# Optimization experiments

Measured on AMD Instinct MI355X. Metric: run time of the kernel, lower is better.

## Reference

```python
import jax, jax.numpy as jnp
import numpy as np

CUTOFF = 5.0
CUTOFF_ANGLE = 3.5
N = 25000
E = 800000
EA = 300000
T = 1600000
NBASIS = 8          # default radial basis size (bessel)
NBASIS_ANG = 8
DIM = 256
DIM_SRC = 64
DIM_DST = 32
DIM_ANGLE = 8
NMAX_ANGLE = 4
SPECIES_DIM = 16
NSPEC = 50


def bessel_basis(r, rc, n):
    # sin(k*pi*r/rc)/r Bessel-type radial basis, k=1..n  -> [E, n]
    x = r[:, None]
    k = jnp.arange(1, n + 1, dtype=r.dtype)[None, :] * (np.pi / rc)
    return jnp.sqrt(2.0 / rc) * jnp.sin(k * x) / x


def tssr2(x):
    # two-sided smooth square-root activation (identity inside |x|<=1)
    ax = jnp.abs(x)
    return jnp.where(ax <= 1.0, x, jnp.sign(x) * (2.0 * jnp.sqrt(jnp.maximum(ax, 1.0)) - 1.0))


def setup_inputs() -> dict:
    key = jax.random.key(0)
    ks = jax.random.split(key, 24)
    species = jax.random.randint(ks[0], (N,), 1, 17)
    edge_src = jax.random.randint(ks[1], (E,), 0, N)
    edge_dst = jax.random.randint(ks[2], (E,), 0, N)
    distances = 0.5 + jax.random.uniform(ks[3], (E,)) * (CUTOFF - 0.5)
    switch = 0.5 + 0.5 * jnp.cos(np.pi * distances / CUTOFF)
    angles = jax.random.uniform(ks[4], (T,)) * np.pi
    angle_src = jax.random.randint(ks[5], (T,), 0, EA)
    angle_dst = jax.random.randint(ks[6], (T,), 0, EA)
    central_atom = jax.random.randint(ks[7], (T,), 0, N)
    distances_angle = 0.5 + jax.random.uniform(ks[8], (EA,)) * (CUTOFF_ANGLE - 0.5)
    switch_angle = 0.5 + 0.5 * jnp.cos(np.pi * distances_angle / CUTOFF_ANGLE)
    s = lambda k, sh, scale: jax.random.normal(k, sh, jnp.float32) * scale
    din0 = SPECIES_DIM + DIM_SRC + NBASIS * DIM_DST + (NMAX_ANGLE + 1) * DIM_ANGLE  # 376
    din1 = DIM + DIM_SRC + NBASIS * DIM_DST + (NMAX_ANGLE + 1) * DIM_ANGLE          # 616
    return {
        'species': species, 'edge_src': edge_src, 'edge_dst': edge_dst,
        'distances': distances, 'switch': switch,
        'angles': angles, 'angle_src': angle_src, 'angle_dst': angle_dst,
        'central_atom': central_atom, 'distances_angle': distances_angle,
        'switch_angle': switch_angle,
        'species_table': s(ks[9], (NSPEC, SPECIES_DIM), 1.0),
        'W_si0': s(ks[10], (SPECIES_DIM, DIM_SRC + DIM_DST), SPECIES_DIM ** -0.5),
        'W_si1': s(ks[11], (DIM, DIM_SRC + DIM_DST), DIM ** -0.5),
        'W_da0': s(ks[12], (NBASIS_ANG, DIM_ANGLE), NBASIS_ANG ** -0.5),
        'W_da1': s(ks[13], (NBASIS_ANG, DIM_ANGLE), NBASIS_ANG ** -0.5),
        'W_mix0': s(ks[14], (din0, DIM), din0 ** -0.5),
        'b_mix0': jnp.zeros((DIM,), jnp.float32),
        'W_mix1': s(ks[15], (din1, DIM), din1 ** -0.5),
        'b_mix1': jnp.zeros((DIM,), jnp.float32),
    }


def reference(species, edge_src, edge_dst, distances, switch, angles, angle_src,
              angle_dst, central_atom, distances_angle, switch_angle,
              species_table, W_si0, W_si1, W_da0, W_da1,
              W_mix0, b_mix0, W_mix1, b_mix1):
    n_atoms = species.shape[0]
    # species encoding (learned/random table lookup)
    xi = species_table[species]                                   # [N, 16]
    # radial embeddings, smoothly switched at cutoff
    rb = bessel_basis(distances, CUTOFF, NBASIS) * switch[:, None]            # [E, 8]
    rba = bessel_basis(distances_angle, CUTOFF_ANGLE, NBASIS_ANG) * switch_angle[:, None]  # [EA, 8]
    # fourier angular features cos(n*theta), n=0..nmax_angle
    nvec = jnp.arange(NMAX_ANGLE + 1, dtype=angles.dtype)[None, :]
    xa = jnp.cos(nvec * angles[:, None])                          # [T, 5]
    for W_si, W_da, W_mix, b_mix in ((W_si0, W_da0, W_mix0, b_mix0),
                                     (W_si1, W_da1, W_mix1, b_mix1)):
        s = xi @ W_si                                             # [N, 96]
        si, si_dst = s[:, :DIM_SRC], s[:, DIM_SRC:]
        # radial message passing: outer(radial_basis, neighbor features) -> scatter-add
        mij = (rb[:, :, None] * si_dst[edge_dst][:, None, :]).reshape(rb.shape[0], -1)  # [E, 256]
        mi = jax.ops.segment_sum(mij, edge_src, num_segments=n_atoms)                   # [N, 256]
        # angular triplet features: pairwise vectors combined per angle
        da = rba @ W_da                                           # [EA, 8]
        dij = da[angle_src] * da[angle_dst]                       # [T, 8]
        ang = (xa[:, :, None] * dij[:, None, :]).reshape(xa.shape[0], -1)               # [T, 40]
        ami = jax.ops.segment_sum(ang, central_atom, num_segments=n_atoms)              # [N, 40]
        # mixing network + tssr2 mixing activation, residual when shapes match
        ei = jnp.concatenate([xi, si, mi, ami], axis=-1)
        dxi = tssr2(ei @ W_mix + b_mix)
        xi = xi + dxi if xi.shape[-1] == dxi.shape[-1] else dxi
    return xi
```

## Files before the change

kernel.cpp:

```cpp
#include <hip/hip_runtime.h>
#include <hip/hip_bf16.h>

typedef __hip_bfloat16 bf16;
typedef __bf16 bf8 __attribute__((ext_vector_type(8)));
typedef float  f4  __attribute__((ext_vector_type(4)));

#define N_ATOMS 25000
#define NE      800000
#define NEA     300000
#define NT      1600000
#define APB     64
#define NBUK    ((N_ATOMS + APB - 1) / APB)
#define PADB    512

#define DIN0  376
#define DIN1  616
#define DINP0 384
#define DINP1 640

#define EBLK ((NE + 4095) / 4096)
#define TBLK ((NT + 4095) / 4096)

#define NFRAG0 ((DINP0 / 32) * 16 * 64)
#define NFRAG1 ((DINP1 / 32) * 16 * 64)
#define NFRAGS (8 * 6 * 64)
#define WBLK   ((NFRAG0 + NFRAG1 + NFRAGS + 255) / 256)

#define S0BLK2 ((N_ATOMS * 120 + 511) / 512)
#define DABLK2 ((NEA + 1 + 511) / 512)

#define MIBLK ((N_ATOMS + 1) / 2)

__device__ __forceinline__ float tssr2f(float x) {
    float ax = fabsf(x);
    return (ax <= 1.f) ? x : copysignf(2.f * __builtin_sqrtf(ax) - 1.f, x);
}

__device__ __forceinline__ unsigned short f2bf_rn(float v) {
    unsigned int b = __float_as_uint(v);
    b += 0x7FFF + ((b >> 16) & 1);
    return (unsigned short)(b >> 16);
}
__device__ __forceinline__ float bf2f(unsigned short u) {
    return __uint_as_float(((unsigned int)u) << 16);
}

__device__ __forceinline__ void wprep_one(const float* __restrict__ W, bf8* __restrict__ Wf,
                                          int K, int N, int ntiles, int f) {
    int lane = f & 63;
    int ft = f >> 6;
    int tile = ft % ntiles;
    int chunk = ft / ntiles;
    int n = tile * 16 + (lane & 15);
    int kb = chunk * 32 + (lane >> 4) * 8;
    bf8 v;
#pragma unroll
    for (int j = 0; j < 8; j++) {
        int k = kb + j;
        v[j] = (__bf16)((k < K) ? W[k * N + n] : 0.f);
    }
    Wf[f] = v;
}

__global__ __launch_bounds__(256) void k_wc(const float* __restrict__ W0, bf8* __restrict__ Wf0,
                                            const float* __restrict__ W1, bf8* __restrict__ Wf1,
                                            const float* __restrict__ WS, bf8* __restrict__ WfS,
                                            const int* __restrict__ esrc, const int* __restrict__ cat,
                                            int* __restrict__ ebcnt, int* __restrict__ tbcnt) {
    int bid = blockIdx.x;
    int t = threadIdx.x;
    if (bid < WBLK) {
        int f = bid * 256 + t;
        if (f < NFRAG0) {
            wprep_one(W0, Wf0, DIN0, 256, 16, f);
        } else if (f < NFRAG0 + NFRAG1) {
            wprep_one(W1, Wf1, DIN1, 256, 16, f - NFRAG0);
        } else if (f < NFRAG0 + NFRAG1 + NFRAGS) {
            wprep_one(WS, WfS, 256, 96, 6, f - NFRAG0 - NFRAG1);
        }
        return;
    }
    bid -= WBLK;
    __shared__ int h[NBUK];
    for (int b = t; b < NBUK; b += 256) h[b] = 0;
    __syncthreads();
    bool isE = bid < EBLK;
    const int* key = isE ? esrc : cat;
    int n = isE ? NE : NT;
    int base = (isE ? bid : bid - EBLK) * 4096;
#pragma unroll
    for (int k = 0; k < 16; k++) {
        int idx = base + k * 256 + t;
        if (idx < n) atomicAdd(&h[key[idx] >> 6], 1);
    }
    __syncthreads();
    int* g = isE ? ebcnt : tbcnt;
    for (int b = t; b < NBUK; b += 256)
        if (h[b]) atomicAdd(&g[b], h[b]);
}

__global__ __launch_bounds__(512) void k_scanB(const int* cnt0, int* off0, int* cur0,
                                               const int* cnt1, int* off1, int* cur1) {
    const int* cnt = blockIdx.x ? cnt1 : cnt0;
    int* off = blockIdx.x ? off1 : off0;
    int* cur = blockIdx.x ? cur1 : cur0;
    __shared__ int sh[512];
    int t = threadIdx.x;
    int v = (t < NBUK) ? cnt[t] : 0;
    sh[t] = v;
    __syncthreads();
    for (int d = 1; d < 512; d <<= 1) {
        int a = (t >= d) ? sh[t - d] : 0;
        __syncthreads();
        sh[t] += a;
        __syncthreads();
    }
    int excl = sh[t] - v;
    if (t <= NBUK) { off[t] = excl; if (t < NBUK) cur[t] = excl; }
}

__global__ __launch_bounds__(512) void k_bpre(const float* __restrict__ eA,
                                              const float* __restrict__ eB,
                                              const int* __restrict__ eC,
                                              const int* __restrict__ ekey,
                                              int* __restrict__ egcur,
                                              float4* __restrict__ ebuk,
                                              const float* __restrict__ tA,
                                              const int* __restrict__ tB,
                                              const int* __restrict__ tC,
                                              const int* __restrict__ tkey,
                                              int* __restrict__ tgcur,
                                              float4* __restrict__ tbuk,
                                              const int* __restrict__ sp,
                                              const float* __restrict__ table,
                                              const float* __restrict__ Wsi,
                                              unsigned short* __restrict__ ei0,
                                              float* __restrict__ sd,
                                              const float* __restrict__ dist,
                                              const float* __restrict__ sw2,
                                              const float* __restrict__ Wda0,
                                              const float* __restrict__ Wda1,
                                              unsigned short* __restrict__ dah0,
                                              unsigned short* __restrict__ dah1) {
    int bid = blockIdx.x;
    int t = threadIdx.x;
    if (bid < EBLK + TBLK) {
        __shared__ int cnt[NBUK];
        __shared__ int rbase[NBUK];
        for (int b = t; b < NBUK; b += 512) cnt[b] = 0;
        __syncthreads();
        bool isE = bid < EBLK;
        const int* key = isE ? ekey : tkey;
        int n = isE ? NE : NT;
        int* gcur = isE ? egcur : tgcur;
        float4* buk = isE ? ebuk : tbuk;
        int base = (isE ? bid : (bid - EBLK)) * 4096;
        float4 pay[8];
        int bk[8], off[8];
#pragma unroll
        for (int k = 0; k < 8; k++) {
            int idx = base + k * 512 + t;
            bk[k] = -1;
            if (idx < n) {
                float4 p;
                if (isE) {
                    p.x = eA[idx];
                    p.y = eB[idx];
                    p.z = __int_as_float(eC[idx]);
                } else {
                    p.x = __cosf(tA[idx]);
                    p.y = __int_as_float(tB[idx]);
                    p.z = __int_as_float(tC[idx]);
                }
                int ky = key[idx];
                p.w = __int_as_float(ky);
                pay[k] = p;
                bk[k] = ky >> 6;
                off[k] = atomicAdd(&cnt[bk[k]], 1);
            }
        }
        __syncthreads();
        for (int b = t; b < NBUK; b += 512)
            if (cnt[b]) rbase[b] = atomicAdd(&gcur[b], cnt[b]);
        __syncthreads();
#pragma unroll
        for (int k = 0; k < 8; k++)
            if (bk[k] >= 0) buk[rbase[bk[k]] + off[k]] = pay[k];
    } else if (bid < EBLK + TBLK + S0BLK2) {
        int idx = (bid - EBLK - TBLK) * 512 + t;
        if (idx >= N_ATOMS * 120) return;
        int i = idx / 120;
        int c = idx - i * 120;
        if (c >= 112) {
            ei0[(size_t)i * DINP0 + 376 + (c - 112)] = 0;
            return;
        }
        int s = sp[i];
        if (c < 16) {
            ei0[(size_t)i * DINP0 + c] = f2bf_rn(table[s * 16 + c]);
        } else {
            int cc = c - 16;
            float acc = 0.f;
#pragma unroll
            for (int k = 0; k < 16; k++)
                acc += table[s * 16 + k] * Wsi[k * 96 + cc];
            if (cc < 64) ei0[(size_t)i * DINP0 + 16 + cc] = f2bf_rn(acc);
            else         sd[i * 32 + cc - 64]             = acc;
        }
    } else {
        int e = (bid - EBLK - TBLK - S0BLK2) * 512 + t;
        if (e > NEA) return;
        if (e == NEA) {
            uint4 z = make_uint4(0, 0, 0, 0);
            *(uint4*)&dah0[(size_t)e * 8] = z;
            *(uint4*)&dah1[(size_t)e * 8] = z;
            return;
        }
        float d = dist[e];
        float s = sw2[e];
        float rb[8];
#pragma unroll
        for (int n = 0; n < 8; n++)
            rb[n] = 0.7559289460f * __sinf((n + 1) * 0.8975979010f * d) / d * s;
        unsigned short h0[8], h1[8];
#pragma unroll
        for (int c = 0; c < 8; c++) {
            float a0 = 0.f, a1 = 0.f;
#pragma unroll
            for (int n = 0; n < 8; n++) {
                a0 += rb[n] * Wda0[n * 8 + c];
                a1 += rb[n] * Wda1[n * 8 + c];
            }
            h0[c] = f2bf_rn(a0);
            h1[c] = f2bf_rn(a1);
        }
        *(uint4*)&dah0[e * 8] = *(uint4*)h0;
        *(uint4*)&dah1[e * 8] = *(uint4*)h1;
    }
}

__global__ __launch_bounds__(256) void k_binB2(const int* __restrict__ ebkoff,
                                               const int* __restrict__ ebcnt,
                                               const float4* __restrict__ ebuk,
                                               float* __restrict__ erb,
                                               int* __restrict__ edi,
                                               int* __restrict__ ebase_g,
                                               int* __restrict__ epcnt_g,
                                               const int* __restrict__ tbkoff,
                                               const int* __restrict__ tbcnt,
                                               const float4* __restrict__ tbuk,
                                               float4* __restrict__ tpay,
                                               int* __restrict__ tbase_g,
                                               int* __restrict__ tpcnt_g) {
    bool isE = blockIdx.x < NBUK;
    int b = isE ? blockIdx.x : (blockIdx.x - NBUK);
    const int* bkoff = isE ? ebkoff : tbkoff;
    const int* bkcnt = isE ? ebcnt : tbcnt;
    const float4* buk = isE ? ebuk : tbuk;
    int* baseg = isE ? ebase_g : tbase_g;
    int* pcntg = isE ? epcnt_g : tpcnt_g;
    int lo = b * APB;
    int hi = min(lo + APB, N_ATOMS);
    int sbase = bkoff[b];
    int bc = bkcnt[b];
    int fb = sbase + b * PADB;
    __shared__ int cntA[APB];
    __shared__ int abase[APB];
    __shared__ int cur[APB];
    int t = threadIdx.x;
    if (t < APB) cntA[t] = 0;
    __syncthreads();
    for (int p = sbase + t; p < sbase + bc; p += 256) {
        int a = __float_as_int(((const float*)(buk + p))[3]);
        atomicAdd(&cntA[a - lo], 1);
    }
    __syncthreads();
    if (t == 0) {
        int run = fb;
        for (int k = 0; k < hi - lo; k++) {
            int pc = (cntA[k] + 7) & ~7;
            abase[k] = run;
            cur[k] = run;
            baseg[lo + k] = run;
            pcntg[lo + k] = pc;
            run += pc;
        }
    }
    __syncthreads();
    if (t < hi - lo) {
        int c = cntA[t];
        int pc = (c + 7) & ~7;
        int base = abase[t];
        if (isE) {
            float4 z = make_float4(0.f, 0.f, 0.f, 0.f);
            for (int s = base + c; s < base + pc; s++) {
                edi[s] = 0;
                *(float4*)&erb[(size_t)s * 8]     = z;
                *(float4*)&erb[(size_t)s * 8 + 4] = z;
            }
        } else {
            float4 pz = make_float4(0.f, __int_as_float(NEA), __int_as_float(NEA), 0.f);
            for (int s = base + c; s < base + pc; s++) tpay[s] = pz;
        }
    }
    __syncthreads();
    for (int p = sbase + t; p < sbase + bc; p += 256) {
        float4 pay = buk[p];
        int a = __float_as_int(pay.w);
        int k = a - lo;
        int slot = atomicAdd(&cur[k], 1);
        if (isE) {
            float d = pay.x, s2 = pay.y;
            float q = 0.6324555320f * s2 / d;
            float r[8];
#pragma unroll
            for (int nn = 0; nn < 8; nn++)
                r[nn] = q * __sinf((nn + 1) * 0.6283185307f * d);
            *(float4*)&erb[(size_t)slot * 8]     = make_float4(r[0], r[1], r[2], r[3]);
            *(float4*)&erb[(size_t)slot * 8 + 4] = make_float4(r[4], r[5], r[6], r[7]);
            edi[slot] = __float_as_int(pay.z);
        } else {
            tpay[slot] = pay;
        }
    }
}

__global__ __launch_bounds__(256) void k_s1(const unsigned short* __restrict__ ei1,
                                            const bf8* __restrict__ Wf,
                                            unsigned short* __restrict__ ei1o,
                                            float* __restrict__ sd) {
    __shared__ __align__(16) __bf16 Asg[4][64][8];
    int t = threadIdx.x;
    int w = t >> 6, lane = t & 63;
    int a0 = blockIdx.x * 64;

    int satom = a0 + (t >> 2);
    int k8 = (t & 3) * 8;
    const unsigned short* arow = &ei1[(size_t)satom * DINP1 + k8];
    bool aok = satom < N_ATOMS;
    int dw = (t >> 2) >> 4;
    int dl = ((t >> 2) & 15) | ((t & 3) << 4);
    __bf16* adst = &Asg[dw][dl][0];

    f4 acc[6];
#pragma unroll
    for (int j = 0; j < 6; j++) {
        f4 z = {0.f, 0.f, 0.f, 0.f};
        acc[j] = z;
    }

    for (int ch = 0; ch < 8; ch++) {
        uint4 v = make_uint4(0, 0, 0, 0);
        if (aok) v = *(const uint4*)(arow + ch * 32);
        __syncthreads();
        *(uint4*)adst = v;
        __syncthreads();
        bf8 afr = *(const bf8*)&Asg[w][lane][0];
        const bf8* wp = &Wf[(ch * 6) * 64 + lane];
#pragma unroll
        for (int tn = 0; tn < 6; tn++) {
            bf8 b = wp[tn * 64];
            acc[tn] = __builtin_amdgcn_mfma_f32_16x16x32_bf16(afr, b, acc[tn], 0, 0, 0);
        }
    }

    int nlo = lane & 15, q = lane >> 4;
#pragma unroll
    for (int r = 0; r < 4; r++) {
        int atom = a0 + w * 16 + q * 4 + r;
        if (atom < N_ATOMS) {
#pragma unroll
            for (int tn = 0; tn < 6; tn++) {
                int col = tn * 16 + nlo;
                float v = acc[tn][r];
                if (col < 64) ei1o[(size_t)atom * DINP1 + 256 + col] = f2bf_rn(v);
                else          sd[atom * 32 + col - 64] = v;
            }
        }
    }
    for (int z = t; z < 64 * 24; z += 256) {
        int za = a0 + z / 24;
        if (za < N_ATOMS) ei1o[(size_t)za * DINP1 + 616 + z % 24] = 0;
    }
}

__device__ __forceinline__ void ami_win(const float4 twA, const unsigned short* __restrict__ dah,
                                        int gmax, int jj, int c,
                                        float& a0, float& a1, float& a2, float& a3, float& a4) {
    float scv[8];
    unsigned short dAv[8], dBv[8];
#pragma unroll
    for (int g = 0; g < 8; g++) {
        if (g < gmax) {
            int sl = g * 8 + jj;
            scv[g] = __shfl(twA.x, sl, 64);
            int ea = __float_as_int(__shfl(twA.y, sl, 64));
            int eb = __float_as_int(__shfl(twA.z, sl, 64));
            dAv[g] = dah[ea * 8 + c];
            dBv[g] = dah[eb * 8 + c];
        }
    }
#pragma unroll
    for (int g = 0; g < 8; g++) {
        if (g < gmax) {
            float dij = bf2f(dAv[g]) * bf2f(dBv[g]);
            float c1 = scv[g];
            float c2 = __builtin_fmaf(2.f * c1, c1, -1.f);
            float c3 = __builtin_fmaf(2.f * c1, c2, -c1);
            float c4 = __builtin_fmaf(2.f * c1, c3, -c2);
            a0 += dij;
            a1 = __builtin_fmaf(c1, dij, a1);
            a2 = __builtin_fmaf(c2, dij, a2);
            a3 = __builtin_fmaf(c3, dij, a3);
            a4 = __builtin_fmaf(c4, dij, a4);
        }
    }
}

__global__ __launch_bounds__(256) void k_seg(const int* __restrict__ ebase,
                                             const int* __restrict__ epcnt,
                                             const float* __restrict__ erb,
                                             const int* __restrict__ edi,
                                             const float* __restrict__ sd,
                                             unsigned short* __restrict__ mo, int mstride,
                                             const int* __restrict__ tbase,
                                             const int* __restrict__ tpcnt,
                                             const float4* __restrict__ tpay,
                                             const unsigned short* __restrict__ dah,
                                             unsigned short* __restrict__ ao, int astride) {
    __shared__ float4 smi[2][64];
    __shared__ float  sam[2][5][8];
    int t = threadIdx.x;
    int wv = t >> 6, l = t & 63;
    int slot = wv >> 1;
    int p    = wv & 1;

    if ((int)blockIdx.x < MIBLK) {
        int i = blockIdx.x * 2 + slot;
        bool valid = (i < N_ATOMS);
        int pbeg = 0, pcnt = 0;
        if (valid) { pbeg = tbase[i]; pcnt = tpcnt[i]; }
        int jj = l >> 3, c = l & 7;
        float a0 = 0.f, a1 = 0.f, a2 = 0.f, a3 = 0.f, a4 = 0.f;

        if (pcnt > 0) {
            int nG = pcnt >> 3;
            if (pcnt <= 128) {
                int h0 = (nG + 1) >> 1;
                int gb = p ? h0 : 0;
                int myg = p ? (nG - h0) : h0;
                if (myg > 0) {
                    int tb = gb * 8;
                    float4 twA = tpay[pbeg + tb + min(l, myg * 8 - 1)];
                    ami_win(twA, dah, myg, jj, c, a0, a1, a2, a3, a4);
                }
            } else {
                int nW = (pcnt + 63) >> 6;
                for (int W = p; W < nW; W += 2) {
                    int wbase = W * 64;
                    int rem = pcnt - wbase;
                    int lim = min(rem, 64);
                    float4 twA = tpay[pbeg + wbase + min(l, rem - 1)];
                    ami_win(twA, dah, lim >> 3, jj, c, a0, a1, a2, a3, a4);
                }
            }
        }

#pragma unroll
        for (int msk = 8; msk <= 32; msk <<= 1) {
            a0 += __shfl_xor(a0, msk, 64);
            a1 += __shfl_xor(a1, msk, 64);
            a2 += __shfl_xor(a2, msk, 64);
            a3 += __shfl_xor(a3, msk, 64);
            a4 += __shfl_xor(a4, msk, 64);
        }
        if (p == 1 && l < 8) {
            sam[slot][0][l] = a0; sam[slot][1][l] = a1; sam[slot][2][l] = a2;
            sam[slot][3][l] = a3; sam[slot][4][l] = a4;
        }
        __syncthreads();
        if (valid && p == 0 && l < 8) {
            a0 += sam[slot][0][l]; a1 += sam[slot][1][l]; a2 += sam[slot][2][l];
            a3 += sam[slot][3][l]; a4 += sam[slot][4][l];
            unsigned short* o = &ao[(size_t)i * astride + c];
            o[0]  = f2bf_rn(a0);
            o[8]  = f2bf_rn(a1);
            o[16] = f2bf_rn(a2);
            o[24] = f2bf_rn(a3);
            o[32] = f2bf_rn(a4);
        }
    } else {
        int i = ((int)blockIdx.x - MIBLK) * 2 + slot;
        bool valid = (i < N_ATOMS);
        int pbeg = 0, pcnt = 0;
        if (valid) { pbeg = ebase[i]; pcnt = epcnt[i]; }
        int n = l >> 3, cb = (l & 7) * 4;
        float4 acc = make_float4(0.f, 0.f, 0.f, 0.f);

        if (pcnt > 0) {
            int nG = pcnt >> 3;
            int h0 = (nG + 1) >> 1;
            int gbeg = p ? h0 : 0;
            int gend = p ? nG : h0;
            if (pcnt <= 64) {
                int eWin = edi[pbeg + min(l, pcnt - 1)];
                if (gbeg < gend) {
                    float cA = erb[((size_t)pbeg + gbeg * 8) * 8 + l];
                    for (int g = gbeg; g < gend; g++) {
                        float4 v[8];
#pragma unroll
                        for (int j = 0; j < 8; j++) {
                            int eid = __shfl(eWin, g * 8 + j, 64);
                            v[j] = *(const float4*)&sd[eid * 32 + cb];
                        }
                        float cB = 0.f;
                        if (g + 1 < gend) cB = erb[((size_t)pbeg + g * 8 + 8) * 8 + l];
#pragma unroll
                        for (int j = 0; j < 8; j++) {
                            float rbj = __shfl(cA, j * 8 + n, 64);
                            acc.x += rbj * v[j].x; acc.y += rbj * v[j].y;
                            acc.z += rbj * v[j].z; acc.w += rbj * v[j].w;
                        }
                        if (g + 1 < gend) cA = cB;
                    }
                }
            } else {
                const int* dp = edi + pbeg;
                for (int g = gbeg; g < gend; g++) {
                    const float* rp = erb + ((size_t)pbeg + g * 8) * 8 + n;
                    float4 v[8];
#pragma unroll
                    for (int j = 0; j < 8; j++) {
                        int eid = dp[g * 8 + j];
                        v[j] = *(const float4*)&sd[eid * 32 + cb];
                    }
#pragma unroll
                    for (int j = 0; j < 8; j++) {
                        float rbj = rp[j * 8];
                        acc.x += rbj * v[j].x; acc.y += rbj * v[j].y;
                        acc.z += rbj * v[j].z; acc.w += rbj * v[j].w;
                    }
                }
            }
        }

        if (p == 1) smi[slot][l] = acc;
        __syncthreads();
        if (valid && p == 0) {
            float4 o = smi[slot][l];
            acc.x += o.x; acc.y += o.y; acc.z += o.z; acc.w += o.w;
            ushort4 pk = make_ushort4(f2bf_rn(acc.x), f2bf_rn(acc.y),
                                      f2bf_rn(acc.z), f2bf_rn(acc.w));
            *(ushort4*)&mo[(size_t)i * mstride + l * 4] = pk;
        }
    }
}

template <int LAYER>
__global__ __launch_bounds__(256) void k_gemm(const unsigned short* __restrict__ ei,
                                              const bf8* __restrict__ Wf,
                                              const float* __restrict__ bias,
                                              const unsigned short* __restrict__ skip,
                                              float* __restrict__ outf,
                                              unsigned short* __restrict__ outb) {
    constexpr int DINP = (LAYER == 0) ? DINP0 : DINP1;
    constexpr int NCH = DINP / 32;
    __shared__ __align__(16) __bf16 Asg[2][64][8];
    int t = threadIdx.x;
    int w = t >> 6, lane = t & 63;
    int a0 = blockIdx.x * 32;

    int f  = t * 4;
    int tA = f >> 9;
    int al = (f >> 3) & 63;
    int j0 = f & 7;
    int sm = al & 15, sq = al >> 4;
    int ga = a0 + tA * 16 + sm;
    const unsigned short* arow = &ei[(size_t)ga * DINP + sq * 8 + j0];
    __bf16* adst = &Asg[0][0][0] + f;
    bool aok = (ga < N_ATOMS);

    f4 acc[2][4];
#pragma unroll
    for (int i = 0; i < 2; i++)
#pragma unroll
        for (int j = 0; j < 4; j++) {
            f4 z = {0.f, 0.f, 0.f, 0.f};
            acc[i][j] = z;
        }

    for (int ch = 0; ch < NCH; ch++) {
        uint2 v = make_uint2(0, 0);
        if (aok) v = *(const uint2*)(arow + ch * 32);
        __syncthreads();
        *(uint2*)adst = v;
        __syncthreads();
        bf8 afr0 = *(const bf8*)&Asg[0][lane][0];
        bf8 afr1 = *(const bf8*)&Asg[1][lane][0];
        const bf8* wp = &Wf[(ch * 16 + w * 4) * 64 + lane];
#pragma unroll
        for (int tn = 0; tn < 4; tn++) {
            bf8 b = wp[tn * 64];
            acc[0][tn] = __builtin_amdgcn_mfma_f32_16x16x32_bf16(afr0, b, acc[0][tn], 0, 0, 0);
            acc[1][tn] = __builtin_amdgcn_mfma_f32_16x16x32_bf16(afr1, b, acc[1][tn], 0, 0, 0);
        }
    }

    int nlo = lane & 15, q = lane >> 4;
#pragma unroll
    for (int tA2 = 0; tA2 < 2; tA2++) {
#pragma unroll
        for (int r = 0; r < 4; r++) {
            int atom = a0 + tA2 * 16 + q * 4 + r;
            if (atom < N_ATOMS) {
#pragma unroll
                for (int tn = 0; tn < 4; tn++) {
                    int col = w * 64 + tn * 16 + nlo;
                    float vv = tssr2f(acc[tA2][tn][r] + bias[col]);
                    if (LAYER == 0) {
                        outb[(size_t)atom * DINP1 + col] = f2bf_rn(vv);
                    } else {
                        outf[(size_t)atom * 256 + col] =
                            vv + bf2f(skip[(size_t)atom * DINP1 + col]);
                    }
                }
            }
        }
    }
}

extern "C" void kernel_launch(void* const* d_in, const int* in_sizes, int n_in,
                              void* d_out, int out_size, void* d_ws, size_t ws_size,
                              hipStream_t stream) {
    const int*   species     = (const int*)d_in[0];
    const int*   edge_src    = (const int*)d_in[1];
    const int*   edge_dst    = (const int*)d_in[2];
    const float* distances   = (const float*)d_in[3];
    const float* sw          = (const float*)d_in[4];
    const float* angles      = (const float*)d_in[5];
    const int*   angle_src   = (const int*)d_in[6];
    const int*   angle_dst   = (const int*)d_in[7];
    const int*   central     = (const int*)d_in[8];
    const float* dist_a      = (const float*)d_in[9];
    const float* sw_a        = (const float*)d_in[10];
    const float* table       = (const float*)d_in[11];
    const float* W_si0       = (const float*)d_in[12];
    const float* W_si1       = (const float*)d_in[13];
    const float* W_da0       = (const float*)d_in[14];
    const float* W_da1       = (const float*)d_in[15];
    const float* W_mix0      = (const float*)d_in[16];
    const float* b_mix0      = (const float*)d_in[17];
    const float* W_mix1      = (const float*)d_in[18];
    const float* b_mix1      = (const float*)d_in[19];
    float* out = (float*)d_out;

    char* p = (char*)d_ws;
    auto alloc = [&](size_t bytes) {
        char* r = p;
        p += (bytes + 255) & ~(size_t)255;
        return (void*)r;
    };
    unsigned short* ei0 = (unsigned short*)alloc((size_t)N_ATOMS * DINP0 * 2);
    unsigned short* ei1 = (unsigned short*)alloc((size_t)N_ATOMS * DINP1 * 2);
    float*  sd   = (float*)alloc((size_t)N_ATOMS * 32 * 4);
    unsigned short* dah0 = (unsigned short*)alloc((size_t)(NEA + 1) * 8 * 2);
    unsigned short* dah1 = (unsigned short*)alloc((size_t)(NEA + 1) * 8 * 2);
    float*  erbf = (float*)alloc((size_t)(NE + NBUK * PADB) * 8 * 4);
    int*    edi  = (int*)alloc((size_t)(NE + NBUK * PADB) * 4);
    float4* tpay = (float4*)alloc((size_t)(NT + NBUK * PADB) * 16);
    float4* ebuk = (float4*)alloc((size_t)NE * 16);
    bf8*    Wf0  = (bf8*)alloc((size_t)NFRAG0 * 16);
    bf8*    Wf1  = (bf8*)alloc((size_t)NFRAG1 * 16);
    bf8*    WfS1 = (bf8*)alloc((size_t)NFRAGS * 16);
    int* ebase  = (int*)alloc((size_t)N_ATOMS * 4);
    int* epcnt  = (int*)alloc((size_t)N_ATOMS * 4);
    int* tbase  = (int*)alloc((size_t)N_ATOMS * 4);
    int* tpcnt  = (int*)alloc((size_t)N_ATOMS * 4);
    int* bcnt   = (int*)alloc((size_t)2 * NBUK * 4);
    int* ebkoff = (int*)alloc((size_t)(NBUK + 1) * 4);
    int* tbkoff = (int*)alloc((size_t)(NBUK + 1) * 4);
    int* gce    = (int*)alloc((size_t)NBUK * 4);
    int* gct    = (int*)alloc((size_t)NBUK * 4);
    (void)ws_size;
    int* ebcnt = bcnt;
    int* tbcnt = bcnt + NBUK;

    float4* tbuk = (float4*)ei1;

    hipMemsetAsync(bcnt, 0, (size_t)2 * NBUK * 4, stream);

    k_wc<<<WBLK + EBLK + TBLK, 256, 0, stream>>>(
        W_mix0, Wf0, W_mix1, Wf1, W_si1, WfS1,
        edge_src, central, ebcnt, tbcnt);

    k_scanB<<<2, 512, 0, stream>>>(ebcnt, ebkoff, gce, tbcnt, tbkoff, gct);

    k_bpre<<<EBLK + TBLK + S0BLK2 + DABLK2, 512, 0, stream>>>(
        distances, sw, edge_dst, edge_src, gce, ebuk,
        angles, angle_src, angle_dst, central, gct, tbuk,
        species, table, W_si0, ei0, sd,
        dist_a, sw_a, W_da0, W_da1, dah0, dah1);

    k_binB2<<<2 * NBUK, 256, 0, stream>>>(
        ebkoff, ebcnt, ebuk, erbf, edi, ebase, epcnt,
        tbkoff, tbcnt, tbuk, tpay, tbase, tpcnt);

    int gemm_grid = (N_ATOMS + 31) / 32;

    k_seg<<<2 * MIBLK, 256, 0, stream>>>(ebase, epcnt, erbf, edi, sd, ei0 + 80, DINP0,
                                         tbase, tpcnt, tpay, dah0, ei0 + 336, DINP0);
    k_gemm<0><<<gemm_grid, 256, 0, stream>>>(ei0, Wf0, b_mix0, nullptr, nullptr, ei1);

    k_s1<<<(N_ATOMS + 63) / 64, 256, 0, stream>>>(ei1, WfS1, ei1, sd);
    k_seg<<<2 * MIBLK, 256, 0, stream>>>(ebase, epcnt, erbf, edi, sd, ei1 + 320, DINP1,
                                         tbase, tpcnt, tpay, dah1, ei1 + 576, DINP1);
    k_gemm<1><<<gemm_grid, 256, 0, stream>>>(ei1, Wf1, b_mix1, ei1, out, nullptr);
}
```

Before: 401.0 us.

## Compute both layers' angular aggregates in one pass with packed triplet payloads

The angular triplet features do not depend on the atom state, so both layers' angular segment sums are now computed in the first segment-reduction launch. The second launch only does the radial part. The two projected angular tables are interleaved into one 32-bit-per-channel array, so each triplet gather fetches both layers at once. Triplet payloads are shrunk from 16 to 8 bytes by packing the two edge indices into bit fields and storing the angle cosine as 24-bit fixed point. This trades a small loss of precision in the cosine and more registers per thread for one fewer pass over the 1.6M triplets and less memory traffic.

```diff
diff --git a/kernel.cpp b/kernel.cpp
--- a/kernel.cpp
+++ b/kernel.cpp
@@ -140,8 +140,7 @@
                                               const float* __restrict__ sw2,
                                               const float* __restrict__ Wda0,
                                               const float* __restrict__ Wda1,
-                                              unsigned short* __restrict__ dah0,
-                                              unsigned short* __restrict__ dah1) {
+                                              unsigned* __restrict__ dah01) {
     int bid = blockIdx.x;
     int t = threadIdx.x;
     if (bid < EBLK + TBLK) {
@@ -212,8 +211,8 @@
         if (e > NEA) return;
         if (e == NEA) {
             uint4 z = make_uint4(0, 0, 0, 0);
-            *(uint4*)&dah0[(size_t)e * 8] = z;
-            *(uint4*)&dah1[(size_t)e * 8] = z;
+            *(uint4*)&dah01[(size_t)e * 8]     = z;
+            *(uint4*)&dah01[(size_t)e * 8 + 4] = z;
             return;
         }
         float d = dist[e];
@@ -222,7 +221,7 @@
 #pragma unroll
         for (int n = 0; n < 8; n++)
             rb[n] = 0.7559289460f * __sinf((n + 1) * 0.8975979010f * d) / d * s;
-        unsigned short h0[8], h1[8];
+        unsigned u[8];
 #pragma unroll
         for (int c = 0; c < 8; c++) {
             float a0 = 0.f, a1 = 0.f;
@@ -231,11 +230,10 @@
                 a0 += rb[n] * Wda0[n * 8 + c];
                 a1 += rb[n] * Wda1[n * 8 + c];
             }
-            h0[c] = f2bf_rn(a0);
-            h1[c] = f2bf_rn(a1);
-        }
-        *(uint4*)&dah0[e * 8] = *(uint4*)h0;
-        *(uint4*)&dah1[e * 8] = *(uint4*)h1;
+            u[c] = (unsigned)f2bf_rn(a0) | ((unsigned)f2bf_rn(a1) << 16);
+        }
+        *(uint4*)&dah01[e * 8]     = *(uint4*)&u[0];
+        *(uint4*)&dah01[e * 8 + 4] = *(uint4*)&u[4];
     }
 }
 
@@ -249,7 +247,7 @@
                                                const int* __restrict__ tbkoff,
                                                const int* __restrict__ tbcnt,
                                                const float4* __restrict__ tbuk,
-                                               float4* __restrict__ tpay,
+                                               uint2* __restrict__ tpay,
                                                int* __restrict__ tbase_g,
                                                int* __restrict__ tpcnt_g) {
     bool isE = blockIdx.x < NBUK;
@@ -299,7 +297,8 @@
                 *(float4*)&erb[(size_t)s * 8 + 4] = z;
             }
         } else {
-            float4 pz = make_float4(0.f, __int_as_float(NEA), __int_as_float(NEA), 0.f);
+            uint2 pz = make_uint2((unsigned)NEA | ((unsigned)NEA << 19),
+                                  ((unsigned)NEA >> 13));
             for (int s = base + c; s < base + pc; s++) tpay[s] = pz;
         }
     }
@@ -320,7 +319,13 @@
             *(float4*)&erb[(size_t)slot * 8 + 4] = make_float4(r[4], r[5], r[6], r[7]);
             edi[slot] = __float_as_int(pay.z);
         } else {
-            tpay[slot] = pay;
+            unsigned ea = (unsigned)__float_as_int(pay.y);
+            unsigned eb = (unsigned)__float_as_int(pay.z);
+            int fx = __float2int_rn(pay.x * 16777216.f);
+            uint2 pk;
+            pk.x = ea | (eb << 19);
+            pk.y = (eb >> 13) | ((unsigned)fx << 6);
+            tpay[slot] = pk;
         }
     }
 }
@@ -384,35 +389,44 @@
     }
 }
 
-__device__ __forceinline__ void ami_win(const float4 twA, const unsigned short* __restrict__ dah,
-                                        int gmax, int jj, int c,
-                                        float& a0, float& a1, float& a2, float& a3, float& a4) {
-    float scv[8];
-    unsigned short dAv[8], dBv[8];
+__device__ __forceinline__ void ami_win2(const uint2 tw, const unsigned* __restrict__ dah01,
+                                         int gmax, int jj, int c,
+                                         float* A0, float* A1) {
+    int fxv[8];
+    unsigned wAv[8], wBv[8];
 #pragma unroll
     for (int g = 0; g < 8; g++) {
         if (g < gmax) {
             int sl = g * 8 + jj;
-            scv[g] = __shfl(twA.x, sl, 64);
-            int ea = __float_as_int(__shfl(twA.y, sl, 64));
-            int eb = __float_as_int(__shfl(twA.z, sl, 64));
-            dAv[g] = dah[ea * 8 + c];
-            dBv[g] = dah[eb * 8 + c];
+            unsigned w0 = (unsigned)__shfl((int)tw.x, sl, 64);
+            unsigned w1 = (unsigned)__shfl((int)tw.y, sl, 64);
+            int ea = (int)(w0 & 0x7FFFFu);
+            int eb = (int)((w0 >> 19) | ((w1 & 0x3Fu) << 13));
+            fxv[g] = ((int)w1) >> 6;
+            wAv[g] = dah01[ea * 8 + c];
+            wBv[g] = dah01[eb * 8 + c];
         }
     }
 #pragma unroll
     for (int g = 0; g < 8; g++) {
         if (g < gmax) {
-            float dij = bf2f(dAv[g]) * bf2f(dBv[g]);
-            float c1 = scv[g];
+            float c1 = (float)fxv[g] * 5.9604644775390625e-8f;
+            float dij0 = __uint_as_float(wAv[g] << 16) * __uint_as_float(wBv[g] << 16);
+            float dij1 = __uint_as_float(wAv[g] & 0xFFFF0000u) *
+                         __uint_as_float(wBv[g] & 0xFFFF0000u);
             float c2 = __builtin_fmaf(2.f * c1, c1, -1.f);
             float c3 = __builtin_fmaf(2.f * c1, c2, -c1);
             float c4 = __builtin_fmaf(2.f * c1, c3, -c2);
-            a0 += dij;
-            a1 = __builtin_fmaf(c1, dij, a1);
-            a2 = __builtin_fmaf(c2, dij, a2);
-            a3 = __builtin_fmaf(c3, dij, a3);
-            a4 = __builtin_fmaf(c4, dij, a4);
+            A0[0] += dij0;
+            A0[1] = __builtin_fmaf(c1, dij0, A0[1]);
+            A0[2] = __builtin_fmaf(c2, dij0, A0[2]);
+            A0[3] = __builtin_fmaf(c3, dij0, A0[3]);
+            A0[4] = __builtin_fmaf(c4, dij0, A0[4]);
+            A1[0] += dij1;
+            A1[1] = __builtin_fmaf(c1, dij1, A1[1]);
+            A1[2] = __builtin_fmaf(c2, dij1, A1[2]);
+            A1[3] = __builtin_fmaf(c3, dij1, A1[3]);
+            A1[4] = __builtin_fmaf(c4, dij1, A1[4]);
         }
     }
 }
@@ -425,23 +439,26 @@
                                              unsigned short* __restrict__ mo, int mstride,
                                              const int* __restrict__ tbase,
                                              const int* __restrict__ tpcnt,
-                                             const float4* __restrict__ tpay,
-                                             const unsigned short* __restrict__ dah,
-                                             unsigned short* __restrict__ ao, int astride) {
+                                             const uint2* __restrict__ tpay,
+                                             const unsigned* __restrict__ dah01,
+                                             unsigned short* __restrict__ ao0, int astride0,
+                                             unsigned short* __restrict__ ao1, int astride1,
+                                             int amiCnt) {
     __shared__ float4 smi[2][64];
-    __shared__ float  sam[2][5][8];
+    __shared__ float  sam[2][10][8];
     int t = threadIdx.x;
     int wv = t >> 6, l = t & 63;
     int slot = wv >> 1;
     int p    = wv & 1;
 
-    if ((int)blockIdx.x < MIBLK) {
+    if ((int)blockIdx.x < amiCnt) {
         int i = blockIdx.x * 2 + slot;
         bool valid = (i < N_ATOMS);
         int pbeg = 0, pcnt = 0;
         if (valid) { pbeg = tbase[i]; pcnt = tpcnt[i]; }
         int jj = l >> 3, c = l & 7;
-        float a0 = 0.f, a1 = 0.f, a2 = 0.f, a3 = 0.f, a4 = 0.f;
+        float A0[5] = {0.f, 0.f, 0.f, 0.f, 0.f};
+        float A1[5] = {0.f, 0.f, 0.f, 0.f, 0.f};
 
         if (pcnt > 0) {
             int nG = pcnt >> 3;
@@ -451,8 +468,8 @@
                 int myg = p ? (nG - h0) : h0;
                 if (myg > 0) {
                     int tb = gb * 8;
-                    float4 twA = tpay[pbeg + tb + min(l, myg * 8 - 1)];
-                    ami_win(twA, dah, myg, jj, c, a0, a1, a2, a3, a4);
+                    uint2 twA = tpay[pbeg + tb + min(l, myg * 8 - 1)];
+                    ami_win2(twA, dah01, myg, jj, c, A0, A1);
                 }
             } else {
                 int nW = (pcnt + 63) >> 6;
@@ -460,37 +477,39 @@
                     int wbase = W * 64;
                     int rem = pcnt - wbase;
                     int lim = min(rem, 64);
-                    float4 twA = tpay[pbeg + wbase + min(l, rem - 1)];
-                    ami_win(twA, dah, lim >> 3, jj, c, a0, a1, a2, a3, a4);
+                    uint2 twA = tpay[pbeg + wbase + min(l, rem - 1)];
+                    ami_win2(twA, dah01, lim >> 3, jj, c, A0, A1);
                 }
             }
         }
 
 #pragma unroll
         for (int msk = 8; msk <= 32; msk <<= 1) {
-            a0 += __shfl_xor(a0, msk, 64);
-            a1 += __shfl_xor(a1, msk, 64);
-            a2 += __shfl_xor(a2, msk, 64);
-            a3 += __shfl_xor(a3, msk, 64);
-            a4 += __shfl_xor(a4, msk, 64);
+#pragma unroll
+            for (int k = 0; k < 5; k++) {
+                A0[k] += __shfl_xor(A0[k], msk, 64);
+                A1[k] += __shfl_xor(A1[k], msk, 64);
+            }
         }
         if (p == 1 && l < 8) {
-            sam[slot][0][l] = a0; sam[slot][1][l] = a1; sam[slot][2][l] = a2;
-            sam[slot][3][l] = a3; sam[slot][4][l] = a4;
+#pragma unroll
+            for (int k = 0; k < 5; k++) {
+                sam[slot][k][l]     = A0[k];
+                sam[slot][k + 5][l] = A1[k];
+            }
         }
         __syncthreads();
         if (valid && p == 0 && l < 8) {
-            a0 += sam[slot][0][l]; a1 += sam[slot][1][l]; a2 += sam[slot][2][l];
-            a3 += sam[slot][3][l]; a4 += sam[slot][4][l];
-            unsigned short* o = &ao[(size_t)i * astride + c];
-            o[0]  = f2bf_rn(a0);
-            o[8]  = f2bf_rn(a1);
-            o[16] = f2bf_rn(a2);
-            o[24] = f2bf_rn(a3);
-            o[32] = f2bf_rn(a4);
+            unsigned short* o0 = &ao0[(size_t)i * astride0 + c];
+            unsigned short* o1 = &ao1[(size_t)i * astride1 + c];
+#pragma unroll
+            for (int k = 0; k < 5; k++) {
+                o0[k * 8] = f2bf_rn(A0[k] + sam[slot][k][l]);
+                o1[k * 8] = f2bf_rn(A1[k] + sam[slot][k + 5][l]);
+            }
         }
     } else {
-        int i = ((int)blockIdx.x - MIBLK) * 2 + slot;
+        int i = ((int)blockIdx.x - amiCnt) * 2 + slot;
         bool valid = (i < N_ATOMS);
         int pbeg = 0, pcnt = 0;
         if (valid) { pbeg = ebase[i]; pcnt = epcnt[i]; }
@@ -663,11 +682,10 @@
     unsigned short* ei0 = (unsigned short*)alloc((size_t)N_ATOMS * DINP0 * 2);
     unsigned short* ei1 = (unsigned short*)alloc((size_t)N_ATOMS * DINP1 * 2);
     float*  sd   = (float*)alloc((size_t)N_ATOMS * 32 * 4);
-    unsigned short* dah0 = (unsigned short*)alloc((size_t)(NEA + 1) * 8 * 2);
-    unsigned short* dah1 = (unsigned short*)alloc((size_t)(NEA + 1) * 8 * 2);
+    unsigned* dah01 = (unsigned*)alloc((size_t)(NEA + 1) * 8 * 4);
     float*  erbf = (float*)alloc((size_t)(NE + NBUK * PADB) * 8 * 4);
     int*    edi  = (int*)alloc((size_t)(NE + NBUK * PADB) * 4);
-    float4* tpay = (float4*)alloc((size_t)(NT + NBUK * PADB) * 16);
+    uint2*  tpay = (uint2*)alloc((size_t)(NT + NBUK * PADB) * 8);
     float4* ebuk = (float4*)alloc((size_t)NE * 16);
     bf8*    Wf0  = (bf8*)alloc((size_t)NFRAG0 * 16);
     bf8*    Wf1  = (bf8*)alloc((size_t)NFRAG1 * 16);
@@ -699,7 +717,7 @@
         distances, sw, edge_dst, edge_src, gce, ebuk,
         angles, angle_src, angle_dst, central, gct, tbuk,
         species, table, W_si0, ei0, sd,
-        dist_a, sw_a, W_da0, W_da1, dah0, dah1);
+        dist_a, sw_a, W_da0, W_da1, dah01);
 
     k_binB2<<<2 * NBUK, 256, 0, stream>>>(
         ebkoff, ebcnt, ebuk, erbf, edi, ebase, epcnt,
@@ -708,11 +726,13 @@
     int gemm_grid = (N_ATOMS + 31) / 32;
 
     k_seg<<<2 * MIBLK, 256, 0, stream>>>(ebase, epcnt, erbf, edi, sd, ei0 + 80, DINP0,
-                                         tbase, tpcnt, tpay, dah0, ei0 + 336, DINP0);
+                                         tbase, tpcnt, tpay, dah01,
+                                         ei0 + 336, DINP0, ei1 + 576, DINP1, MIBLK);
     k_gemm<0><<<gemm_grid, 256, 0, stream>>>(ei0, Wf0, b_mix0, nullptr, nullptr, ei1);
 
     k_s1<<<(N_ATOMS + 63) / 64, 256, 0, stream>>>(ei1, WfS1, ei1, sd);
-    k_seg<<<2 * MIBLK, 256, 0, stream>>>(ebase, epcnt, erbf, edi, sd, ei1 + 320, DINP1,
-                                         tbase, tpcnt, tpay, dah1, ei1 + 576, DINP1);
+    k_seg<<<MIBLK, 256, 0, stream>>>(ebase, epcnt, erbf, edi, sd, ei1 + 320, DINP1,
+                                     tbase, tpcnt, tpay, dah01,
+                                     ei1 + 576, DINP1, ei1 + 576, DINP1, 0);
     k_gemm<1><<<gemm_grid, 256, 0, stream>>>(ei1, Wf1, b_mix1, ei1, out, nullptr);
 }
```

New measurement: 373.6 us. 6.8% less time.
